# Kernel optimization log

Hardware: AMD Instinct MI355X
Metric: run time of the kernel (lower is better)

The kernel has to match this reference:

```python
import jax, jax.numpy as jnp
import numpy as np

B, S, IN_F, OUT_F = 4, 2048, 4096, 4096
LUT_SIZE = 256


def setup_inputs() -> dict:
    key = jax.random.key(0)
    k_x, k_idx = jax.random.split(key, 2)
    x = jax.random.normal(k_x, (B, S, IN_F), dtype=jnp.float32)
    # quantized weight codes, one per weight element (uint8 in torch; int32 here)
    grid_indices = jax.random.randint(k_idx, (OUT_F, IN_F), 0, LUT_SIZE, dtype=jnp.int32)
    # per-output-row scale, initialized to ones as in the module
    scale = jnp.ones((OUT_F, 1), dtype=jnp.float32)
    # PRIMAL_LUT: 256-entry linear manifold codebook
    lut = jnp.linspace(-1.0, 1.0, LUT_SIZE, dtype=jnp.float32)
    return {"x": x, "grid_indices": grid_indices, "scale": scale, "lut": lut}


def reference(x, grid_indices, scale, lut):
    # dequant: gather codebook entries per weight element, scale per output row
    weights = lut[grid_indices] * scale            # [OUT_F, IN_F]
    # F.linear(x, weights) == x @ weights.T
    return jnp.einsum('bsi,oi->bso', x, weights)   # [B, S, OUT_F]
```

## Files before the change

### kernel.cpp

```cpp
#include <hip/hip_runtime.h>
#include <hip/hip_bf16.h>


#define M_DIM 8192
#define N_DIM 4096
#define K_DIM 4096
#define BM 256
#define BN 256
#define BK 64
#define NKT (K_DIM / BK)

typedef __bf16 bf16x8 __attribute__((ext_vector_type(8)));
typedef float floatx4 __attribute__((ext_vector_type(4)));
typedef int intx4 __attribute__((ext_vector_type(4)));
typedef unsigned short ushortx8 __attribute__((ext_vector_type(8)));

__device__ __forceinline__ unsigned short f2bf(float f) {
    return __builtin_bit_cast(unsigned short, (__bf16)f);
}

__device__ __forceinline__ void async_load16(const void* g, void* l) {
    auto gp = reinterpret_cast<const __attribute__((address_space(1))) void*>(
        reinterpret_cast<unsigned long long>(g));
    auto lp = reinterpret_cast<__attribute__((address_space(3))) void*>(
        static_cast<unsigned int>(reinterpret_cast<unsigned long long>(l)));
    __builtin_amdgcn_global_load_lds(gp, lp, 16, 0, 0);
}

__global__ __launch_bounds__(256) void prep(const float* __restrict__ x,
                                            unsigned short* __restrict__ xb,
                                            const int* __restrict__ idx,
                                            const float* __restrict__ scale,
                                            const float* __restrict__ lut,
                                            unsigned short* __restrict__ wb) {
    __shared__ float slut[256];
    if (blockIdx.x < 16384) {
        size_t i = ((size_t)blockIdx.x * 256 + threadIdx.x) * 8;
        floatx4 a = __builtin_nontemporal_load((const floatx4*)(x + i));
        floatx4 b = __builtin_nontemporal_load((const floatx4*)(x + i + 4));
        ushortx8 v;
        v[0] = f2bf(a[0]); v[1] = f2bf(a[1]); v[2] = f2bf(a[2]); v[3] = f2bf(a[3]);
        v[4] = f2bf(b[0]); v[5] = f2bf(b[1]); v[6] = f2bf(b[2]); v[7] = f2bf(b[3]);
        *(ushortx8*)(xb + i) = v;
    } else {
        if (threadIdx.x < 256) slut[threadIdx.x] = lut[threadIdx.x];
        __syncthreads();
        size_t i = ((size_t)(blockIdx.x - 16384) * 256 + threadIdx.x) * 8;
        int row = (int)(i >> 12);
        float s = scale[row];
        intx4 i0 = __builtin_nontemporal_load((const intx4*)(idx + i));
        intx4 i1 = __builtin_nontemporal_load((const intx4*)(idx + i + 4));
        ushortx8 v;
        v[0] = f2bf(slut[i0[0]] * s); v[1] = f2bf(slut[i0[1]] * s);
        v[2] = f2bf(slut[i0[2]] * s); v[3] = f2bf(slut[i0[3]] * s);
        v[4] = f2bf(slut[i1[0]] * s); v[5] = f2bf(slut[i1[1]] * s);
        v[6] = f2bf(slut[i1[2]] * s); v[7] = f2bf(slut[i1[3]] * s);
        *(ushortx8*)(wb + i) = v;
    }
}


#define SBAR() __builtin_amdgcn_sched_barrier(0)
#define BARRIER()                          \
    do {                                   \
        asm volatile("" ::: "memory");     \
        __builtin_amdgcn_s_barrier();      \
        asm volatile("" ::: "memory");     \
    } while (0)
#define VMCNT4() asm volatile("s_waitcnt vmcnt(4)" ::: "memory")

#define MMA(HM, HN, BR)                                                          \
    do {                                                                         \
        __builtin_amdgcn_s_setprio(1);                                           \
        _Pragma("unroll") for (int mt = 0; mt < 4; mt++)                         \
            _Pragma("unroll") for (int nt = 0; nt < 2; nt++)                     \
                _Pragma("unroll") for (int ks = 0; ks < 2; ks++)                 \
                    acc[(HM) * 4 + mt][(HN) * 2 + nt] =                          \
                        __builtin_amdgcn_mfma_f32_16x16x32_bf16(                 \
                            aReg[mt][ks], BR[nt][ks],                            \
                            acc[(HM) * 4 + mt][(HN) * 2 + nt], 0, 0, 0);         \
        __builtin_amdgcn_s_setprio(0);                                           \
    } while (0)

__global__ __launch_bounds__(512, 2) void gemm256(const unsigned short* __restrict__ A,
                                                  const unsigned short* __restrict__ Bw,
                                                  float* __restrict__ C) {
    extern __shared__ unsigned short lds[];
    unsigned short* __restrict__ As = lds;
    unsigned short* __restrict__ Bs = lds + 2 * BM * BK;

    const int id = blockIdx.x;
    const int wg = (id & 7) * 64 + (id >> 3);
    const int m0 = (wg >> 4) * BM;
    const int n0 = (wg & 15) * BN;

    const int t    = threadIdx.x;
    const int lane = t & 63;
    const int w    = t >> 6;
    const int wm   = w >> 2;
    const int wn   = w & 3;
    const int quad = lane >> 4;
    const int lcol = lane & 15;

    const int sRow = t >> 3;
    const int gOff = (((t & 7) - sRow) & 7) * 8;

    floatx4 acc[8][4];
#pragma unroll
    for (int i = 0; i < 8; i++)
#pragma unroll
        for (int j = 0; j < 4; j++) acc[i][j] = (floatx4)0.0f;

    bf16x8 aReg[4][2], b0Reg[2][2], b1Reg[2][2];

    auto stageA = [&](int buf, int half, int kt) {
        const int ko = (kt & (NKT - 1)) * BK + gOff;
#pragma unroll
        for (int c = 0; c < 2; c++) {
            int r = c * 128 + half * 64 + sRow;
            const unsigned short* s = A + (size_t)(m0 + r) * K_DIM + ko;
            unsigned short* d = As + buf * (BM * BK) + r * BK + (t & 7) * 8;
            async_load16(s, d);
        }
    };
    auto stageB = [&](int buf, int half, int kt) {
        const int ko = (kt & (NKT - 1)) * BK + gOff;
#pragma unroll
        for (int c = 0; c < 2; c++) {
            int r = c * 128 + ((sRow >> 5) * 64) + half * 32 + (sRow & 31);
            const unsigned short* s = Bw + (size_t)(n0 + r) * K_DIM + ko;
            unsigned short* d = Bs + buf * (BN * BK) + r * BK + (t & 7) * 8;
            async_load16(s, d);
        }
    };

    auto lda = [&](int buf, int hm) {
#pragma unroll
        for (int mt = 0; mt < 4; mt++) {
            int R = wm * 128 + hm * 64 + mt * 16 + lcol;
#pragma unroll
            for (int ks = 0; ks < 2; ks++) {
                int ch = (ks * 4 + quad + R) & 7;
                aReg[mt][ks] = *(const bf16x8*)(As + buf * (BM * BK) + R * BK + ch * 8);
            }
        }
    };
    auto ldb = [&](bf16x8(&bR)[2][2], int buf, int hn) {
#pragma unroll
        for (int nt = 0; nt < 2; nt++) {
            int R = wn * 64 + hn * 32 + nt * 16 + lcol;
#pragma unroll
            for (int ks = 0; ks < 2; ks++) {
                int ch = (ks * 4 + quad + R) & 7;
                bR[nt][ks] = *(const bf16x8*)(Bs + buf * (BN * BK) + R * BK + ch * 8);
            }
        }
    };

    stageA(0, 0, 0); stageB(0, 0, 0);
    stageA(0, 1, 0); stageB(0, 1, 0);
    stageA(1, 0, 1); stageB(1, 0, 1);
    VMCNT4();
    BARRIER();
    SBAR();

    for (int i = 0; i < NKT / 2; i++) {
        const int T0 = 2 * i;
        lda(0, 0); ldb(b0Reg, 0, 0);
        stageA(1, 1, T0 + 1);
        SBAR(); BARRIER();
        MMA(0, 0, b0Reg);
        SBAR(); BARRIER(); SBAR();
        ldb(b1Reg, 0, 1);
        stageB(1, 1, T0 + 1);
        SBAR(); BARRIER();
        MMA(0, 1, b1Reg);
        SBAR(); BARRIER(); SBAR();
        lda(0, 1);
        stageA(0, 0, T0 + 2);
        SBAR(); BARRIER();
        MMA(1, 0, b0Reg);
        SBAR(); BARRIER(); SBAR();
        stageB(0, 0, T0 + 2);
        SBAR(); BARRIER();
        MMA(1, 1, b1Reg);
        SBAR(); VMCNT4(); BARRIER(); SBAR();
        lda(1, 0); ldb(b0Reg, 1, 0);
        stageA(0, 1, T0 + 2);
        SBAR(); BARRIER();
        MMA(0, 0, b0Reg);
        SBAR(); BARRIER(); SBAR();
        ldb(b1Reg, 1, 1);
        stageB(0, 1, T0 + 2);
        SBAR(); BARRIER();
        MMA(0, 1, b1Reg);
        SBAR(); BARRIER(); SBAR();
        lda(1, 1);
        stageA(1, 0, T0 + 3);
        SBAR(); BARRIER();
        MMA(1, 0, b0Reg);
        SBAR(); BARRIER(); SBAR();
        stageB(1, 0, T0 + 3);
        SBAR(); BARRIER();
        MMA(1, 1, b1Reg);
        SBAR(); VMCNT4(); BARRIER(); SBAR();
    }

#pragma unroll
    for (int mt = 0; mt < 8; mt++) {
#pragma unroll
        for (int r = 0; r < 4; r++) {
            int row = m0 + wm * 128 + mt * 16 + quad * 4 + r;
            float* cr = C + (size_t)row * N_DIM + n0 + wn * 64 + lcol;
#pragma unroll
            for (int nt = 0; nt < 4; nt++)
                __builtin_nontemporal_store(acc[mt][nt][r], cr + nt * 16);
        }
    }
}

__global__ __launch_bounds__(256) void gemm_fallback(const float* __restrict__ x,
                                                     const int* __restrict__ idx,
                                                     const float* __restrict__ scale,
                                                     const float* __restrict__ lut,
                                                     float* __restrict__ C) {
    __shared__ float xs[16][17];
    __shared__ float wsm[16][17];
    const int tx = threadIdx.x & 15;
    const int ty = threadIdx.x >> 4;
    const int m = blockIdx.y * 16 + ty;
    const int n = blockIdx.x * 16 + tx;
    float acc = 0.f;
    for (int k0 = 0; k0 < K_DIM; k0 += 16) {
        xs[ty][tx] = x[(size_t)m * K_DIM + k0 + tx];
        int wrow = blockIdx.x * 16 + ty;
        wsm[ty][tx] = lut[idx[(size_t)wrow * K_DIM + k0 + tx]] * scale[wrow];
        __syncthreads();
#pragma unroll
        for (int kk = 0; kk < 16; kk++) acc += xs[ty][kk] * wsm[tx][kk];
        __syncthreads();
    }
    C[(size_t)m * N_DIM + n] = acc;
}

extern "C" void kernel_launch(void* const* d_in, const int* in_sizes, int n_in,
                              void* d_out, int out_size, void* d_ws, size_t ws_size,
                              hipStream_t stream) {
    const float* x     = (const float*)d_in[0];
    const int*   gidx  = (const int*)d_in[1];
    const float* scale = (const float*)d_in[2];
    const float* lut   = (const float*)d_in[3];
    float*       out   = (float*)d_out;

    const size_t needA = (size_t)M_DIM * K_DIM * sizeof(unsigned short);
    const size_t needW = (size_t)N_DIM * K_DIM * sizeof(unsigned short);

    if (ws_size >= needA + needW) {
        static bool s_attr = false;
        if (!s_attr) {
            (void)hipFuncSetAttribute((const void*)gemm256,
                                      hipFuncAttributeMaxDynamicSharedMemorySize,
                                      131072);
            s_attr = true;
        }
        unsigned short* Ab = (unsigned short*)d_ws;
        unsigned short* Wb = Ab + (size_t)M_DIM * K_DIM;
        prep<<<24576, 256, 0, stream>>>(x, Ab, gidx, scale, lut, Wb);
        gemm256<<<(M_DIM / BM) * (N_DIM / BN), 512, 131072, stream>>>(Ab, Wb, out);
    } else {
        dim3 grid(N_DIM / 16, M_DIM / 16);
        gemm_fallback<<<grid, 16 * 16, 0, stream>>>(x, gidx, scale, lut, out);
    }
}
```

Before: 472.8 us.

## Restructure GEMM main loop into k-slice register ping-pong with fewer barriers

Splits each 64-wide K tile into two k-slices and double-buffers the A and B fragments in registers (aA/aB, bA/bB), so LDS reads for the next slice are issued before the current 16-MFMA block runs. The barrier count per step drops, and the global-to-LDS staging order and wait points change to vmcnt(0). The goal is to hide LDS latency behind MFMA work and cut synchronisation overhead. The stricter vmcnt(0) waits and the reordered staging add risk of stalls or of buffer hazards, and the register-buffered fragments may raise register pressure.

```diff
diff --git a/kernel.cpp b/kernel.cpp
--- a/kernel.cpp
+++ b/kernel.cpp
@@ -67,20 +67,7 @@
         __builtin_amdgcn_s_barrier();      \
         asm volatile("" ::: "memory");     \
     } while (0)
-#define VMCNT4() asm volatile("s_waitcnt vmcnt(4)" ::: "memory")
-
-#define MMA(HM, HN, BR)                                                          \
-    do {                                                                         \
-        __builtin_amdgcn_s_setprio(1);                                           \
-        _Pragma("unroll") for (int mt = 0; mt < 4; mt++)                         \
-            _Pragma("unroll") for (int nt = 0; nt < 2; nt++)                     \
-                _Pragma("unroll") for (int ks = 0; ks < 2; ks++)                 \
-                    acc[(HM) * 4 + mt][(HN) * 2 + nt] =                          \
-                        __builtin_amdgcn_mfma_f32_16x16x32_bf16(                 \
-                            aReg[mt][ks], BR[nt][ks],                            \
-                            acc[(HM) * 4 + mt][(HN) * 2 + nt], 0, 0, 0);         \
-        __builtin_amdgcn_s_setprio(0);                                           \
-    } while (0)
+#define VMCNT0() asm volatile("s_waitcnt vmcnt(0)" ::: "memory")
 
 __global__ __launch_bounds__(512, 2) void gemm256(const unsigned short* __restrict__ A,
                                                   const unsigned short* __restrict__ Bw,
@@ -111,7 +98,7 @@
 #pragma unroll
         for (int j = 0; j < 4; j++) acc[i][j] = (floatx4)0.0f;
 
-    bf16x8 aReg[4][2], b0Reg[2][2], b1Reg[2][2];
+    bf16x8 aA[4], aB[4], bA[4], bB[4];
 
     auto stageA = [&](int buf, int half, int kt) {
         const int ko = (kt & (NKT - 1)) * BK + gOff;
@@ -134,76 +121,97 @@
         }
     };
 
-    auto lda = [&](int buf, int hm) {
+    auto ldA = [&](bf16x8(&dst)[4], int buf, int hm, int ks) {
 #pragma unroll
         for (int mt = 0; mt < 4; mt++) {
             int R = wm * 128 + hm * 64 + mt * 16 + lcol;
-#pragma unroll
-            for (int ks = 0; ks < 2; ks++) {
-                int ch = (ks * 4 + quad + R) & 7;
-                aReg[mt][ks] = *(const bf16x8*)(As + buf * (BM * BK) + R * BK + ch * 8);
-            }
-        }
-    };
-    auto ldb = [&](bf16x8(&bR)[2][2], int buf, int hn) {
-#pragma unroll
-        for (int nt = 0; nt < 2; nt++) {
-            int R = wn * 64 + hn * 32 + nt * 16 + lcol;
-#pragma unroll
-            for (int ks = 0; ks < 2; ks++) {
-                int ch = (ks * 4 + quad + R) & 7;
-                bR[nt][ks] = *(const bf16x8*)(Bs + buf * (BN * BK) + R * BK + ch * 8);
-            }
-        }
-    };
-
-    stageA(0, 0, 0); stageB(0, 0, 0);
-    stageA(0, 1, 0); stageB(0, 1, 0);
-    stageA(1, 0, 1); stageB(1, 0, 1);
-    VMCNT4();
+            int ch = (ks * 4 + quad + R) & 7;
+            dst[mt] = *(const bf16x8*)(As + buf * (BM * BK) + R * BK + ch * 8);
+        }
+    };
+    auto ldB = [&](bf16x8(&dst)[4], int buf, int ks) {
+#pragma unroll
+        for (int nt = 0; nt < 4; nt++) {
+            int R = wn * 64 + nt * 16 + lcol;
+            int ch = (ks * 4 + quad + R) & 7;
+            dst[nt] = *(const bf16x8*)(Bs + buf * (BN * BK) + R * BK + ch * 8);
+        }
+    };
+
+    auto MMA16 = [&](bf16x8(&a)[4], bf16x8(&b)[4], int hm) {
+        __builtin_amdgcn_s_setprio(1);
+#pragma unroll
+        for (int mt = 0; mt < 4; mt++)
+#pragma unroll
+            for (int nt = 0; nt < 4; nt++)
+                acc[hm * 4 + mt][nt] = __builtin_amdgcn_mfma_f32_16x16x32_bf16(
+                    a[mt], b[nt], acc[hm * 4 + mt][nt], 0, 0, 0);
+        __builtin_amdgcn_s_setprio(0);
+    };
+
+    stageA(0, 0, 0); stageA(0, 1, 0);
+    stageB(0, 0, 0); stageB(0, 1, 0);
+    stageB(1, 0, 1);
+    VMCNT0();
     BARRIER();
+    ldA(aA, 0, 0, 0);
+    ldB(bA, 0, 0);
     SBAR();
 
     for (int i = 0; i < NKT / 2; i++) {
         const int T0 = 2 * i;
-        lda(0, 0); ldb(b0Reg, 0, 0);
+        stageA(1, 0, T0 + 1); stageB(1, 1, T0 + 1);
+        BARRIER();
+        ldA(aB, 0, 1, 0);
+        SBAR();
+        MMA16(aA, bA, 0);
+        SBAR();
         stageA(1, 1, T0 + 1);
-        SBAR(); BARRIER();
-        MMA(0, 0, b0Reg);
-        SBAR(); BARRIER(); SBAR();
-        ldb(b1Reg, 0, 1);
-        stageB(1, 1, T0 + 1);
-        SBAR(); BARRIER();
-        MMA(0, 1, b1Reg);
-        SBAR(); BARRIER(); SBAR();
-        lda(0, 1);
-        stageA(0, 0, T0 + 2);
-        SBAR(); BARRIER();
-        MMA(1, 0, b0Reg);
-        SBAR(); BARRIER(); SBAR();
+        BARRIER();
+        ldA(aA, 0, 1, 1);
+        ldB(bB, 0, 1);
+        SBAR();
+        MMA16(aB, bA, 1);
+        SBAR();
+        BARRIER();
+        ldA(aB, 0, 0, 1);
+        SBAR();
+        MMA16(aA, bB, 1);
+        SBAR();
+        VMCNT0();
         stageB(0, 0, T0 + 2);
-        SBAR(); BARRIER();
-        MMA(1, 1, b1Reg);
-        SBAR(); VMCNT4(); BARRIER(); SBAR();
-        lda(1, 0); ldb(b0Reg, 1, 0);
+        BARRIER();
+        ldA(aA, 1, 0, 0);
+        ldB(bA, 1, 0);
+        SBAR();
+        MMA16(aB, bB, 0);
+        SBAR();
+        stageA(0, 0, T0 + 2); stageB(0, 1, T0 + 2);
+        BARRIER();
+        ldA(aB, 1, 1, 0);
+        SBAR();
+        MMA16(aA, bA, 0);
+        SBAR();
         stageA(0, 1, T0 + 2);
-        SBAR(); BARRIER();
-        MMA(0, 0, b0Reg);
-        SBAR(); BARRIER(); SBAR();
-        ldb(b1Reg, 1, 1);
-        stageB(0, 1, T0 + 2);
-        SBAR(); BARRIER();
-        MMA(0, 1, b1Reg);
-        SBAR(); BARRIER(); SBAR();
-        lda(1, 1);
-        stageA(1, 0, T0 + 3);
-        SBAR(); BARRIER();
-        MMA(1, 0, b0Reg);
-        SBAR(); BARRIER(); SBAR();
+        BARRIER();
+        ldA(aA, 1, 1, 1);
+        ldB(bB, 1, 1);
+        SBAR();
+        MMA16(aB, bA, 1);
+        SBAR();
+        BARRIER();
+        ldA(aB, 1, 0, 1);
+        SBAR();
+        MMA16(aA, bB, 1);
+        SBAR();
+        VMCNT0();
         stageB(1, 0, T0 + 3);
-        SBAR(); BARRIER();
-        MMA(1, 1, b1Reg);
-        SBAR(); VMCNT4(); BARRIER(); SBAR();
+        BARRIER();
+        ldA(aA, 0, 0, 0);
+        ldB(bA, 0, 0);
+        SBAR();
+        MMA16(aB, bB, 0);
+        SBAR();
     }
 
 #pragma unroll
```

Measured after the change: 588.0 us. 1.24x slower.
